# Performance work log

Hardware: AMD Instinct MI355X
Metric: run time of the kernel (lower is better)

The kernel has to match this reference:

```python
import jax, jax.numpy as jnp
import numpy as np
from itertools import combinations

WIRES, LAYERS, CUTOFF, OUT_WIRES, BATCH = 4, 2, 10, 3, 2048

def _annih(c):
    # annihilation operator a in the Fock basis, truncated to cutoff c
    return jnp.diag(jnp.sqrt(jnp.arange(1, c, dtype=jnp.float32)), 1).astype(jnp.complex64)

_expm = jnp.vectorize(jax.scipy.linalg.expm, signature='(n,n)->(n,n)')

def _squeeze(r, phi, a):
    # S(z) = exp((z* a^2 - z a+^2)/2), z = r e^{i phi}; r, phi have arbitrary batch shape
    z = (r * jnp.exp(1j * phi)).astype(jnp.complex64)[..., None, None]
    a2 = a @ a
    ad2 = a.conj().T @ a.conj().T
    return _expm(0.5 * (jnp.conj(z) * a2 - z * ad2))

def _disp(r, phi, a):
    # D(alpha) = exp(alpha a+ - alpha* a), alpha = r e^{i phi}
    al = (r * jnp.exp(1j * phi)).astype(jnp.complex64)[..., None, None]
    ad = a.conj().T
    return _expm(al * ad - jnp.conj(al) * a)

def _bs(theta, phi, a):
    # SF BSgate: B = exp(theta (e^{i phi} a b+ - e^{-i phi} a+ b))
    ad = a.conj().T
    G = theta * (jnp.exp(1j * phi) * jnp.kron(a, ad) - jnp.exp(-1j * phi) * jnp.kron(ad, a))
    return jax.scipy.linalg.expm(G.astype(jnp.complex64))

def _cx(s, a):
    # SF CXgate: exp(-i s x1 p2 / hbar) = exp(-(s/2) (a+a+) kron (b-b+)) with hbar=2
    ad = a.conj().T
    G = (-s / 2.0) * jnp.kron(a + ad, a - ad)
    return jax.scipy.linalg.expm(G.astype(jnp.complex64))

def _apply1(state, U, m):
    # apply single-mode gate U ([c,c] shared or [B,c,c] per-sample) to mode m
    if U.ndim == 2:
        return jnp.moveaxis(jnp.tensordot(state, U, axes=[[1 + m], [1]]), -1, 1 + m)
    st = jnp.moveaxis(state, 1 + m, -1)
    st = jnp.einsum('b...j,bij->b...i', st, U)
    return jnp.moveaxis(st, -1, 1 + m)

def _apply2(state, U4, m1, m2):
    # apply two-mode gate U4 [c,c,c,c] (out1,out2,in1,in2) to modes (m1, m2)
    st = jnp.moveaxis(state, (1 + m1, 1 + m2), (-2, -1))
    st = jnp.einsum('b...kl,ijkl->b...ij', st, U4)
    return jnp.moveaxis(st, (-2, -1), (1 + m1, 1 + m2))

def _forward(jets, s_scale, disp_mag, disp_phase, squeeze_mag, squeeze_phase, w_dense, b_dense):
    B, c = jets.shape[0], CUTOFF
    a = _annih(c)
    eta, phi, pt = jets[:, :, 0], jets[:, :, 1], jets[:, :, 2]  # each [B, WIRES]
    scale = 10.0 / (1.0 + jnp.exp(-s_scale)) + 0.01
    # vacuum |0...0> for every sample
    state = jnp.zeros((B,) + (c,) * WIRES, jnp.complex64)
    state = state.at[(slice(None),) + (0,) * WIRES].set(1.0)
    # per-sample data-encoding gates
    S_enc = _squeeze(eta, pt * phi / 2.0, a)      # [B, WIRES, c, c]
    D_enc = _disp(scale * pt, eta, a)             # [B, WIRES, c, c]
    for w in range(WIRES):
        state = _apply1(state, S_enc[:, w], w)
        state = _apply1(state, D_enc[:, w], w)
    # fixed entangling gates (shared across batch)
    CX = _cx(1.0, a).reshape(c, c, c, c)
    BS = _bs(jnp.pi / 4.0, jnp.pi / 2.0, a).reshape(c, c, c, c)
    # learned per-layer single-mode gates (shared across batch)
    S_lay = _squeeze(squeeze_mag, squeeze_phase, a)  # [LAYERS, WIRES, c, c]
    D_lay = _disp(disp_mag, disp_phase, a)
    for L in range(LAYERS):
        for (i, j) in combinations(range(WIRES), 2):
            state = _apply2(state, CX, i, j)
        for i in range(WIRES):
            state = _apply2(state, BS, i, (i + 1) % WIRES)
        for w in range(WIRES):
            state = _apply1(state, S_lay[L, w], w)
            state = _apply1(state, D_lay[L, w], w)
    probs = jnp.abs(state) ** 2
    nvec = jnp.arange(c, dtype=jnp.float32)
    photons = jnp.stack(
        [probs.sum(axis=tuple(1 + k for k in range(WIRES) if k != m)) @ nvec
         for m in range(OUT_WIRES)], axis=1)  # [B, OUT_WIRES] mean photon numbers
    return (photons @ w_dense + b_dense)[:, 0]  # [B]

def setup_inputs() -> dict:
    key = jax.random.key(0)
    ks = jax.random.split(key, 8)
    u = lambda k, sh: jax.random.uniform(k, sh, jnp.float32, -1.0, 1.0)
    return {
        'jets': 0.3 * jax.random.normal(ks[0], (BATCH, WIRES, 3), jnp.float32),
        's_scale': u(ks[1], ()),
        'disp_mag': u(ks[2], (LAYERS, WIRES)),
        'disp_phase': u(ks[3], (LAYERS, WIRES)),
        'squeeze_mag': u(ks[4], (LAYERS, WIRES)),
        'squeeze_phase': u(ks[5], (LAYERS, WIRES)),
        'w_dense': u(ks[6], (OUT_WIRES, 1)),
        'b_dense': jnp.zeros((1,), jnp.float32),
    }

def reference(jets, s_scale, disp_mag, disp_phase, squeeze_mag, squeeze_phase, w_dense, b_dense):
    return _forward(jets, s_scale, disp_mag, disp_phase, squeeze_mag, squeeze_phase, w_dense, b_dense)
```

## Files before the change

kernel.cpp:

```cpp
#include <hip/hip_runtime.h>
#include <math.h>


namespace {

constexpr int NTB = 1024;
constexpr int SMEM_STATE = 162352;
constexpr double THETA = 0.7853981633974483096;

struct cxf { float x, y; };
typedef float v2f __attribute__((ext_vector_type(2)));
typedef float v4f __attribute__((ext_vector_type(4)));

constexpr int U_OFF = 15872;

__device__ __forceinline__ cxf gen_squeeze_f(int i, int j, float zr, float zi){
  if (j == i+2){ float g = 0.5f*sqrtf((float)((i+1)*(i+2))); return {zr*g, -zi*g}; }
  if (i == j+2){ float g = 0.5f*sqrtf((float)((j+1)*(j+2))); return {-zr*g, -zi*g}; }
  return {0.f, 0.f};
}
__device__ __forceinline__ cxf gen_disp_f(int i, int j, float ar, float ai){
  if (i == j+1){ float g = sqrtf((float)i); return {ar*g, ai*g}; }
  if (j == i+1){ float g = sqrtf((float)j); return {-ar*g, ai*g}; }
  return {0.f, 0.f};
}

__device__ void expm_f32(bool act, int n, cxf* M, cxf* P, cxf* T, cxf* R, int lane){
  const int n2 = n*n;
  if (act){
    for (int e=lane; e<n2; e+=64){ M[e].x *= 0x1p-10f; M[e].y *= 0x1p-10f; }
    for (int e=lane; e<n2; e+=64){
      P[e] = M[e];
      cxf r = M[e];
      if (e % (n+1) == 0) r.x += 1.f;
      R[e] = r;
    }
  }
  __syncthreads();
  for (int t=2; t<=12; ++t){
    if (act){
      float inv = 1.f/(float)t;
      for (int e=lane; e<n2; e+=64){
        int i = e/n, j = e - i*n;
        float ax=0.f, ay=0.f;
        for (int k=0;k<n;k++){
          cxf p = P[i*n+k], m = M[k*n+j];
          ax += p.x*m.x - p.y*m.y;
          ay += p.x*m.y + p.y*m.x;
        }
        T[e] = {ax*inv, ay*inv};
      }
    }
    __syncthreads();
    { cxf* tmp = P; P = T; T = tmp; }
    if (act){ for (int e=lane; e<n2; e+=64){ R[e].x += P[e].x; R[e].y += P[e].y; } }
    __syncthreads();
  }
  for (int s=0; s<10; ++s){
    if (act){
      for (int e=lane; e<n2; e+=64){
        int i = e/n, j = e - i*n;
        float ax=0.f, ay=0.f;
        for (int k=0;k<n;k++){
          cxf p = R[i*n+k], q = R[k*n+j];
          ax += p.x*q.x - p.y*q.y;
          ay += p.x*q.y + p.y*q.x;
        }
        T[e] = {ax, ay};
      }
    }
    __syncthreads();
    { cxf* tmp = R; R = T; T = tmp; }
    __syncthreads();
  }
}

__global__ __launch_bounds__(256)
void gates_kernel(const float* __restrict__ dmag, const float* __restrict__ dphase,
                  const float* __restrict__ smag, const float* __restrict__ sphase,
                  float* __restrict__ wsf){
  __shared__ double lam[10];
  __shared__ float scr[4][4][200];
  const int tid = threadIdx.x;
  const int wv = tid >> 6, lane = tid & 63, g = blockIdx.x;
  float* ws_V  = wsf;
  float* ws_VT = wsf + 100;
  float* ws_W  = wsf + 200;
  cxf* ws_BS   = (cxf*)(wsf + 1200);
  cxf* ws_stage= (cxf*)(wsf + 6600);

  if (tid < 10){
    double lo = -6.0, hi = 6.0;
    for (int it=0; it<80; ++it){
      double mid = 0.5*(lo+hi);
      int cnt = 0; double q = 1.0;
      for (int i=0;i<10;i++){
        q = -mid - (i ? (double)i/q : 0.0);
        if (fabs(q) < 1e-300) q = -1e-300;
        if (q < 0.0) cnt++;
      }
      if (cnt > tid) hi = mid; else lo = mid;
    }
    double x = 0.5*(lo+hi);
    double p[10];
    p[0] = 1.0; p[1] = x;
    for (int k=1;k<9;k++) p[k+1] = (x*p[k] - sqrt((double)k)*p[k-1]) * (1.0/sqrt((double)(k+1)));
    double nn=0.0; for (int k=0;k<10;k++) nn += p[k]*p[k];
    double inv = 1.0/sqrt(nn);
    lam[tid] = x;
    if (g == 0){
      for (int k=0;k<10;k++){
        float v = (float)(p[k]*inv);
        ws_V[k*10+tid]  = v;
        ws_VT[tid*10+k] = v;
      }
    }
  }
  __syncthreads();

  int t = g*4 + wv;
  bool act = (t < 45);
  int n = 10, bn = 0, ilo = 0;
  if (act && t >= 10 && t < 29){
    bn = t - 10; ilo = bn < 10 ? 0 : bn - 9;
    int ihi = bn < 10 ? bn : 9;
    n = ihi - ilo + 1;
  }
  cxf* M = (cxf*)scr[wv][0];
  cxf* P = (cxf*)scr[wv][1];
  cxf* T = (cxf*)scr[wv][2];
  cxf* R = (cxf*)scr[wv][3];
  if (act){
    if (t < 10){
      float l = (float)lam[t];
      for (int e=lane; e<100; e+=64){
        int i=e/10, j=e-10*i;
        float v = 0.f;
        if (j == i+1) v = -0.5f*l*sqrtf((float)(i+1));
        else if (i == j+1) v = 0.5f*l*sqrtf((float)i);
        M[e] = {v, 0.f};
      }
    } else if (t < 29){
      for (int e=lane; e<n*n; e+=64){
        int rr=e/n, c=e-n*rr;
        float v = 0.f;
        if (c == rr+1) v = (float)THETA*sqrtf((float)((ilo+rr+1)*(bn-ilo-rr)));
        else if (rr == c+1) v = (float)THETA*sqrtf((float)((ilo+c+1)*(bn-ilo-c)));
        M[e] = {0.f, v};
      }
    } else {
      int idx = t-29, kind = idx>>3, L=(idx>>2)&1, w=idx&3;
      float r_ = kind ? dmag[L*4+w]   : smag[L*4+w];
      float ph = kind ? dphase[L*4+w] : sphase[L*4+w];
      float zr = r_*cosf(ph), zi = r_*sinf(ph);
      for (int e=lane; e<100; e+=64){
        int i=e/10, j=e-10*i;
        M[e] = kind ? gen_disp_f(i,j,zr,zi) : gen_squeeze_f(i,j,zr,zi);
      }
    }
  }
  __syncthreads();
  expm_f32(act, n, M, P, T, R, lane);
  if (act){
    if (t < 10){
      for (int e=lane;e<100;e+=64){
        int i=e/10, j=e-10*i;
        ws_W[t*100 + j*10 + i] = R[e].x;
      }
    } else if (t < 29){
      for (int e=lane;e<100;e+=64){
        int rr=e/10, c=e-10*rr;
        cxf o; o.x=0.f; o.y=0.f;
        if (rr < n && c < n) o = R[rr*n+c];
        ws_BS[bn*100 + c*10 + rr] = o;
      }
    } else {
      int idx = t-29;
      for (int e=lane;e<100;e+=64) ws_stage[idx*100 + e] = R[e];
    }
  }
}

__global__ __launch_bounds__(512)
void fuse_kernel(float* __restrict__ wsf){
  __shared__ cxf ulraw[8][100];
  const int tid = threadIdx.x, wv = tid>>6, lane = tid&63;
  const cxf* stage = (const cxf*)(wsf + 6600);
  cxf* ws_UL = (cxf*)(wsf + 5000);
  cxf* ws_WU = (cxf*)(wsf + 9800);
  const float* V  = wsf;
  const float* Wt = wsf + 200;
  const cxf* Sm = stage + wv*100;
  const cxf* Dm = stage + (8+wv)*100;
  for (int e=lane; e<100; e+=64){
    int i=e/10, j=e-10*i;
    float ax=0.f, ay=0.f;
    for (int k=0;k<10;k++){
      cxf d=Dm[i*10+k], s=Sm[k*10+j];
      ax += d.x*s.x - d.y*s.y;
      ay += d.x*s.y + d.y*s.x;
    }
    ulraw[wv][e] = {ax, ay};
  }
  __syncthreads();
  cxf t0={0.f,0.f}, t1={0.f,0.f};
  if (wv == 0){
    {
      int e=lane, i=e/10, j=e-10*i;
      float ox=0.f, oy=0.f;
      for (int k=0;k<10;k++){ float v=V[k*10+i]; ox+=v*ulraw[0][k*10+j].x; oy+=v*ulraw[0][k*10+j].y; }
      t0 = {ox, oy};
    }
    if (lane+64 < 100){
      int e=lane+64, i=e/10, j=e-10*i;
      float ox=0.f, oy=0.f;
      for (int k=0;k<10;k++){ float v=V[k*10+i]; ox+=v*ulraw[0][k*10+j].x; oy+=v*ulraw[0][k*10+j].y; }
      t1 = {ox, oy};
    }
  }
  __syncthreads();
  if (wv == 0){
    ulraw[0][lane] = t0;
    if (lane+64 < 100) ulraw[0][lane+64] = t1;
  }
  __syncthreads();
  for (int e=tid; e<400; e+=512){
    int fi = e/100, r = e-100*fi;
    int f = (fi==0) ? 0 : (3+fi);
    int i=r/10, j=r-10*i;
    ws_UL[f*100 + j*10 + i] = ulraw[f][i*10+j];
  }
  for (int round=0; round<4; ++round){
    int id = round*8 + wv;
    if (id < 30){
      int b = 1 + id/10, n = id - (id/10)*10;
      const cxf* Ub = ulraw[b];
      for (int e=lane; e<100; e+=64){
        int i=e/10, j=e-10*i;
        float ax=0.f, ay=0.f;
        for (int k=0;k<10;k++){
          float w = Wt[n*100 + k*10 + i];
          ax += w*Ub[k*10+j].x;
          ay += w*Ub[k*10+j].y;
        }
        cxf o; o.x=ax; o.y=ay;
        ws_WU[id*100 + j*10 + i] = o;
      }
    }
  }
}

__global__ __launch_bounds__(128)
void enc_kernel(const float* __restrict__ jets, const float* __restrict__ sscale,
                float* __restrict__ wsf){
  __shared__ float scr[2][4][200];
  __shared__ cxf col[10];
  __shared__ cxf uacc[10];
  const int tid = threadIdx.x, wv = tid>>6, lane = tid&63;
  const int blk = blockIdx.x, b = blk>>2, w = blk&3;

  float eta = jets[b*12 + w*3 + 0];
  float jph = jets[b*12 + w*3 + 1];
  float pt  = jets[b*12 + w*3 + 2];

  cxf* M = (cxf*)scr[wv][0];
  cxf* P = (cxf*)scr[wv][1];
  cxf* T = (cxf*)scr[wv][2];
  cxf* R = (cxf*)scr[wv][3];
  {
    float zr, zi;
    if (wv == 0){ float phs = pt*jph*0.5f; zr = eta*cosf(phs); zi = eta*sinf(phs); }
    else {
      double sc = 10.0/(1.0 + exp(-(double)sscale[0])) + 0.01;
      float mag = (float)sc*pt; zr = mag*cosf(eta); zi = mag*sinf(eta);
    }
    for (int e=lane; e<100; e+=64){
      int i=e/10, j=e-10*i;
      M[e] = wv ? gen_disp_f(i,j,zr,zi) : gen_squeeze_f(i,j,zr,zi);
    }
  }
  __syncthreads();
  expm_f32(true, 10, M, P, T, R, lane);
  cxf* Rs = (cxf*)scr[0][3];
  cxf* Rd = (cxf*)scr[1][3];
  if (tid < 10) col[tid] = Rs[tid*10];
  __syncthreads();
  if (tid < 10){
    float ax=0.f, ay=0.f;
    for (int k=0;k<10;k++){
      cxf d = Rd[tid*10+k], c = col[k];
      ax += d.x*c.x - d.y*c.y;
      ay += d.x*c.y + d.y*c.x;
    }
    uacc[tid] = {ax, ay};
  }
  __syncthreads();
  if (tid < 10){
    float rx, ry;
    if (w == 0){
      rx = 0.f; ry = 0.f;
      for (int k=0;k<10;k++){
        float v = wsf[k*10 + tid];
        rx += v*uacc[k].x;
        ry += v*uacc[k].y;
      }
    } else { rx = uacc[tid].x; ry = uacc[tid].y; }
    float* u_out = wsf + U_OFF + (b*40 + w*10 + tid)*2;
    u_out[0] = rx;
    u_out[1] = ry;
  }
}

__device__ __forceinline__ constexpr int WS(int w){
  return w==0 ? 1010 : (w==1 ? 101 : (w==2 ? 10 : 1));
}

#define DECL_ACC4 \
  v4f a0={0.f,0.f,0.f,0.f}, a1=a0, a2=a0, a3=a0, a4=a0, \
      a5=a0, a6=a0, a7=a0, a8=a0, a9=a0;

#define LDS_RD10 \
  v4f r0=S[base], r1=S[base+sm], r2=S[base+2*sm], r3=S[base+3*sm], r4=S[base+4*sm], \
      r5=S[base+5*sm], r6=S[base+6*sm], r7=S[base+7*sm], r8=S[base+8*sm], r9=S[base+9*sm];

#define CE(i,ur,ui) \
  a##i = __builtin_elementwise_fma((v4f){(ur),(ur),(ur),(ur)}, vv, a##i); \
  a##i = __builtin_elementwise_fma((v4f){-(ui),(ui),-(ui),(ui)}, vs, a##i);
#define RE(i,u) a##i = __builtin_elementwise_fma((v4f){(u),(u),(u),(u)}, vv, a##i);

#define CSTEP(rk,krow) { \
  const v4f* Up = (const v4f*)(U + (krow)*10); \
  v4f q0=Up[0],q1=Up[1],q2=Up[2],q3=Up[3],q4=Up[4]; \
  v4f vv=rk, vs=__builtin_shufflevector(rk,rk,1,0,3,2); \
  CE(0,q0.x,q0.y) CE(1,q0.z,q0.w) CE(2,q1.x,q1.y) CE(3,q1.z,q1.w) \
  CE(4,q2.x,q2.y) CE(5,q2.z,q2.w) CE(6,q3.x,q3.y) CE(7,q3.z,q3.w) \
  CE(8,q4.x,q4.y) CE(9,q4.z,q4.w) }
#define CSTEP_ALL CSTEP(r0,0) CSTEP(r1,1) CSTEP(r2,2) CSTEP(r3,3) CSTEP(r4,4) \
  CSTEP(r5,5) CSTEP(r6,6) CSTEP(r7,7) CSTEP(r8,8) CSTEP(r9,9)

#define RSTEP2(ra_,rb_,krow) { \
  const v4f* Mp = (const v4f*)(Mt + (krow)*10); \
  v4f q0=Mp[0],q1=Mp[1],q2=Mp[2],q3=Mp[3],q4=Mp[4]; \
  { v4f vv=ra_; RE(0,q0.x) RE(1,q0.y) RE(2,q0.z) RE(3,q0.w) RE(4,q1.x) \
                RE(5,q1.y) RE(6,q1.z) RE(7,q1.w) RE(8,q2.x) RE(9,q2.y) } \
  { v4f vv=rb_; RE(0,q2.z) RE(1,q2.w) RE(2,q3.x) RE(3,q3.y) RE(4,q3.z) \
                RE(5,q3.w) RE(6,q4.x) RE(7,q4.y) RE(8,q4.z) RE(9,q4.w) } }
#define RSTEP_ALL RSTEP2(r0,r1,0) RSTEP2(r2,r3,2) RSTEP2(r4,r5,4) \
  RSTEP2(r6,r7,6) RSTEP2(r8,r9,8)

#define PST4(i) { S[base + (i)*sm] = a##i; }
#define PALL4 PST4(0) PST4(1) PST4(2) PST4(3) PST4(4) PST4(5) PST4(6) PST4(7) PST4(8) PST4(9)
#define BSTQ(r) if ((r) < sz){ S[wadr] = a##r; wadr += ds; }
#define BSTQ_ALL BSTQ(0) BSTQ(1) BSTQ(2) BSTQ(3) BSTQ(4) BSTQ(5) BSTQ(6) BSTQ(7) BSTQ(8) BSTQ(9)

__device__ __forceinline__ void apply1_c4(v4f* S, const cxf* __restrict__ U, int m, int tid){
  const int sm = WS(m);
  const int x0 = (m==0)?1:0, x1=(m<=1)?2:1, x2=(m<=2)?3:2;
  const int s0 = WS(x0), s1 = WS(x1), s2 = WS(x2);
  if (tid < 1000){
    int c0=tid/100, rem=tid-100*c0, c1=rem/10, c2=rem-10*c1;
    int base = c0*s0 + c1*s1 + c2*s2;
    LDS_RD10
    DECL_ACC4
    CSTEP_ALL
    PALL4
  }
}

__device__ __forceinline__ void apply1_r4(v4f* S, const float* __restrict__ Mt, int m, int tid){
  const int sm = WS(m);
  const int x0 = (m==0)?1:0, x1=(m<=1)?2:1, x2=(m<=2)?3:2;
  const int s0 = WS(x0), s1 = WS(x1), s2 = WS(x2);
  if (tid < 1000){
    int c0=tid/100, rem=tid-100*c0, c1=rem/10, c2=rem-10*c1;
    int base = c0*s0 + c1*s1 + c2*s2;
    LDS_RD10
    DECL_ACC4
    RSTEP_ALL
    PALL4
  }
}

__device__ __forceinline__ void applyW4(v4f* S, const float* __restrict__ Wall, int m1, int m2, int tid){
  const int sm  = WS(m2);
  const int sm1 = WS(m1);
  int ra=-1, rb=-1;
  for (int q=0;q<4;q++) if (q!=m1 && q!=m2){ if (ra<0) ra=q; else rb=q; }
  const int sa = WS(ra), sb = WS(rb);
  if (tid < 1000){
    int n = tid/100, rem = tid-100*n, qa = rem/10, qb = rem-10*qa;
    int base = n*sm1 + qa*sa + qb*sb;
    const float* __restrict__ Mt = Wall + n*100;
    LDS_RD10
    DECL_ACC4
    RSTEP_ALL
    PALL4
  }
}

__device__ __forceinline__ void applyWU4(v4f* S, const cxf* __restrict__ WUall, int m2, int tid){
  const int sm = WS(m2);
  const int ra = (m2==1)?2:1;
  const int rb = (m2==3)?2:3;
  const int sa = WS(ra), sb = WS(rb);
  if (tid < 1000){
    int n = tid/100, rem = tid-100*n, qa = rem/10, qb = rem-10*qa;
    int base = n*WS(0) + qa*sa + qb*sb;
    const cxf* __restrict__ U = WUall + n*100;
    LDS_RD10
    DECL_ACC4
    CSTEP_ALL
    PALL4
  }
}

__device__ __forceinline__ v2f measure14(const v4f* S, const cxf* __restrict__ U, int m, int tid){
  const int sm = WS(m);
  const int x0 = (m==0)?1:0, x1=(m<=1)?2:1, x2=3;
  const int s0 = WS(x0), s1 = WS(x1), s2 = WS(x2);
  v2f s = {0.f, 0.f};
  if (tid < 1000){
    int c0=tid/100, rem=tid-100*c0, c1=rem/10, c2=rem-10*c1;
    int base = c0*s0 + c1*s1 + c2*s2;
    LDS_RD10
    DECL_ACC4
    CSTEP_ALL
    #define MQ4(i) { s.x += (float)(i)*(a##i.x*a##i.x + a##i.y*a##i.y); \
                     s.y += (float)(i)*(a##i.z*a##i.z + a##i.w*a##i.w); }
    MQ4(1) MQ4(2) MQ4(3) MQ4(4) MQ4(5) MQ4(6) MQ4(7) MQ4(8) MQ4(9)
    #undef MQ4
  }
  return s;
}

__device__ __forceinline__ void applyBS4(v4f* S, const cxf* __restrict__ BSp, int m1, int m2, int tid){
  int ra=-1, rb=-1;
  for (int q=0;q<4;q++) if (q!=m1 && q!=m2){ if (ra<0) ra=q; else rb=q; }
  const int sa = WS(ra), sb = WS(rb);
  const int s1 = WS(m1), s2 = WS(m2);
  const int ds = s1 - s2;
  #pragma unroll 1
  for (int w0=0; w0<2048; w0+=NTB){
    int it = w0 + tid;
    if (it < 1900){
      int bn = it/100, rest = it-100*bn;
      int ilo = bn<10?0:bn-9, ihi = bn<10?bn:9, sz = ihi-ilo+1;
      int ca = rest/10, cb = rest-10*ca;
      int base = ca*sa + cb*sb;
      const cxf* __restrict__ Bt = BSp + bn*100;
      DECL_ACC4
      int radr = base + ilo*s1 + (bn-ilo)*s2;
      int kk = 0;
      #pragma unroll 1
      for (int c=0;c<sz;c++){
        v4f vv = S[radr];
        v4f vs = __builtin_shufflevector(vv, vv, 1, 0, 3, 2);
        const v4f* Bp = (const v4f*)(Bt + kk);
        v4f q0=Bp[0],q1=Bp[1],q2=Bp[2],q3=Bp[3],q4=Bp[4];
        CE(0,q0.x,q0.y) CE(1,q0.z,q0.w) CE(2,q1.x,q1.y) CE(3,q1.z,q1.w)
        CE(4,q2.x,q2.y) CE(5,q2.z,q2.w) CE(6,q3.x,q3.y) CE(7,q3.z,q3.w)
        CE(8,q4.x,q4.y) CE(9,q4.z,q4.w)
        radr += ds; kk += 10;
      }
      int wadr = base + ilo*s1 + (bn-ilo)*s2;
      BSTQ_ALL
    }
  }
}

__global__ __launch_bounds__(NTB)
__attribute__((amdgpu_waves_per_eu(4)))
void state_kernel(const float* __restrict__ wd, const float* __restrict__ bd,
                  const float* __restrict__ wsf, float* __restrict__ out){
  extern __shared__ __align__(16) char smem[];
  v4f* S    = (v4f*)smem;
  cxf* uv   = (cxf*)(smem + 161584);
  v2f* red  = (v2f*)(smem + 162224);

  const float* __restrict__ V   = wsf;
  const float* __restrict__ VT  = wsf + 100;
  const float* __restrict__ W   = wsf + 200;
  const cxf*   __restrict__ BSm = (const cxf*)(wsf + 1200);
  const cxf*   __restrict__ UL  = (const cxf*)(wsf + 5000);
  const cxf*   __restrict__ WU  = (const cxf*)(wsf + 9800);
  const cxf*   __restrict__ uw  = (const cxf*)(wsf + U_OFF);

  const int tid = threadIdx.x, wv = tid>>6, lane = tid&63;
  const int b = blockIdx.x;

  if (tid < 80) uv[tid] = uw[b*80 + tid];
  __syncthreads();

  for (int e=tid; e<10000; e+=NTB){
    int c0=e/1000, r_=e-1000*c0, c1=r_/100, r2_=r_-100*c1, c2=r2_/10, c3=r2_-10*c2;
    cxf A0 = uv[c0],    B0 = uv[10+c1], C0 = uv[20+c2], D0 = uv[30+c3];
    cxf A1 = uv[40+c0], B1 = uv[50+c1], C1 = uv[60+c2], D1 = uv[70+c3];
    float pr = A0.x*B0.x - A0.y*B0.y, pi = A0.x*B0.y + A0.y*B0.x;
    float qr = pr*C0.x - pi*C0.y,  qi = pr*C0.y + pi*C0.x;
    float e0r = qr*D0.x - qi*D0.y, e0i = qr*D0.y + qi*D0.x;
    pr = A1.x*B1.x - A1.y*B1.y; pi = A1.x*B1.y + A1.y*B1.x;
    qr = pr*C1.x - pi*C1.y;  qi = pr*C1.y + pi*C1.x;
    float e1r = qr*D1.x - qi*D1.y, e1i = qr*D1.y + qi*D1.x;
    S[c0*1010 + c1*101 + c2*10 + c3] = (v4f){e0r, e0i, e1r, e1i};
  }
  __syncthreads();

  applyW4(S, W, 0, 1, tid); __syncthreads();
  applyW4(S, W, 0, 2, tid); __syncthreads();
  applyW4(S, W, 0, 3, tid); __syncthreads();
  apply1_r4(S, VT, 0, tid); __syncthreads();
  apply1_r4(S, V, 1, tid);  __syncthreads();
  applyW4(S, W, 1, 2, tid); __syncthreads();
  applyW4(S, W, 1, 3, tid); __syncthreads();
  apply1_r4(S, VT, 1, tid); __syncthreads();
  apply1_r4(S, V, 2, tid);  __syncthreads();
  applyW4(S, W, 2, 3, tid); __syncthreads();
  apply1_r4(S, VT, 2, tid); __syncthreads();
  applyBS4(S, BSm, 0, 1, tid); __syncthreads();
  applyBS4(S, BSm, 1, 2, tid); __syncthreads();
  applyBS4(S, BSm, 2, 3, tid); __syncthreads();
  applyBS4(S, BSm, 3, 0, tid); __syncthreads();
  apply1_c4(S, UL, 0, tid); __syncthreads();

  applyWU4(S, WU,        1, tid); __syncthreads();
  applyWU4(S, WU + 1000, 2, tid); __syncthreads();
  applyWU4(S, WU + 2000, 3, tid); __syncthreads();
  apply1_r4(S, VT, 0, tid); __syncthreads();
  apply1_r4(S, V, 1, tid);  __syncthreads();
  applyW4(S, W, 1, 2, tid); __syncthreads();
  applyW4(S, W, 1, 3, tid); __syncthreads();
  apply1_r4(S, VT, 1, tid); __syncthreads();
  apply1_r4(S, V, 2, tid);  __syncthreads();
  applyW4(S, W, 2, 3, tid); __syncthreads();
  apply1_r4(S, VT, 2, tid); __syncthreads();
  applyBS4(S, BSm, 0, 1, tid); __syncthreads();
  applyBS4(S, BSm, 1, 2, tid); __syncthreads();
  applyBS4(S, BSm, 2, 3, tid); __syncthreads();
  applyBS4(S, BSm, 3, 0, tid); __syncthreads();

  float w0 = wd[0], w1 = wd[1], w2 = wd[2];
  v2f m0 = measure14(S, UL + 400, 0, tid);
  v2f m1 = measure14(S, UL + 500, 1, tid);
  v2f m2 = measure14(S, UL + 600, 2, tid);
  v2f acc;
  acc.x = w0*m0.x + w1*m1.x + w2*m2.x;
  acc.y = w0*m0.y + w1*m1.y + w2*m2.y;

  for (int off=32; off; off>>=1){
    acc.x += __shfl_down(acc.x, off, 64);
    acc.y += __shfl_down(acc.y, off, 64);
  }
  if (lane == 0) red[wv] = acc;
  __syncthreads();
  if (tid == 0){
    float sx = 0.f, sy = 0.f;
    for (int i=0;i<16;i++){ sx += red[i].x; sy += red[i].y; }
    out[2*b+0] = sx + bd[0];
    out[2*b+1] = sy + bd[0];
  }
}

}

extern "C" void kernel_launch(void* const* d_in, const int* in_sizes, int n_in,
                              void* d_out, int out_size, void* d_ws, size_t ws_size,
                              hipStream_t stream){
  const float* jets   = (const float*)d_in[0];
  const float* sscale = (const float*)d_in[1];
  const float* dmag   = (const float*)d_in[2];
  const float* dphase = (const float*)d_in[3];
  const float* smag   = (const float*)d_in[4];
  const float* sphase = (const float*)d_in[5];
  const float* wd     = (const float*)d_in[6];
  const float* bd     = (const float*)d_in[7];
  float* out = (float*)d_out;
  float* wsf = (float*)d_ws;
  int B = in_sizes[0] / 12;

  (void)hipFuncSetAttribute(reinterpret_cast<const void*>(&state_kernel),
                            hipFuncAttributeMaxDynamicSharedMemorySize, SMEM_STATE);

  gates_kernel<<<12, 256, 0, stream>>>(dmag, dphase, smag, sphase, wsf);
  fuse_kernel<<<1, 512, 0, stream>>>(wsf);
  enc_kernel<<<B*4, 128, 0, stream>>>(jets, sscale, wsf);
  state_kernel<<<B/2, NTB, SMEM_STATE, stream>>>(wd, bd, wsf, out);
}
```

Measured before the change: 856.7 us.

## Halve block size and give each thread two state fibers

After: 930.4 us. 1.09x slower.

```diff
diff --git a/kernel.cpp b/kernel.cpp
--- a/kernel.cpp
+++ b/kernel.cpp
@@ -4,7 +4,7 @@
 
 namespace {
 
-constexpr int NTB = 1024;
+constexpr int NTB = 512;
 constexpr int SMEM_STATE = 162352;
 constexpr double THETA = 0.7853981633974483096;
 
@@ -315,55 +315,108 @@
   return w==0 ? 1010 : (w==1 ? 101 : (w==2 ? 10 : 1));
 }
 
-#define DECL_ACC4 \
-  v4f a0={0.f,0.f,0.f,0.f}, a1=a0, a2=a0, a3=a0, a4=a0, \
-      a5=a0, a6=a0, a7=a0, a8=a0, a9=a0;
-
-#define LDS_RD10 \
-  v4f r0=S[base], r1=S[base+sm], r2=S[base+2*sm], r3=S[base+3*sm], r4=S[base+4*sm], \
-      r5=S[base+5*sm], r6=S[base+6*sm], r7=S[base+7*sm], r8=S[base+8*sm], r9=S[base+9*sm];
-
-#define CE(i,ur,ui) \
+#define SHUF4(v) __builtin_shufflevector(v, v, 1, 0, 3, 2)
+
+#define DECL_A \
+  v4f a0={0.f,0.f,0.f,0.f}, a1=a0, a2=a0, a3=a0, a4=a0, a5=a0, a6=a0, a7=a0, a8=a0, a9=a0;
+#define DECL_B \
+  v4f b0={0.f,0.f,0.f,0.f}, b1=b0, b2=b0, b3=b0, b4=b0, b5=b0, b6=b0, b7=b0, b8=b0, b9=b0;
+
+#define CE_A(i,ur,ui) \
   a##i = __builtin_elementwise_fma((v4f){(ur),(ur),(ur),(ur)}, vv, a##i); \
   a##i = __builtin_elementwise_fma((v4f){-(ui),(ui),-(ui),(ui)}, vs, a##i);
-#define RE(i,u) a##i = __builtin_elementwise_fma((v4f){(u),(u),(u),(u)}, vv, a##i);
-
-#define CSTEP(rk,krow) { \
+#define CE_B(i,ur,ui) \
+  b##i = __builtin_elementwise_fma((v4f){(ur),(ur),(ur),(ur)}, vv, b##i); \
+  b##i = __builtin_elementwise_fma((v4f){-(ui),(ui),-(ui),(ui)}, vs, b##i);
+#define RE_A(i,u) a##i = __builtin_elementwise_fma((v4f){(u),(u),(u),(u)}, vv, a##i);
+#define RE_B(i,u) b##i = __builtin_elementwise_fma((v4f){(u),(u),(u),(u)}, vv, b##i);
+
+#define CROW_A CE_A(0,q0.x,q0.y) CE_A(1,q0.z,q0.w) CE_A(2,q1.x,q1.y) CE_A(3,q1.z,q1.w) \
+  CE_A(4,q2.x,q2.y) CE_A(5,q2.z,q2.w) CE_A(6,q3.x,q3.y) CE_A(7,q3.z,q3.w) \
+  CE_A(8,q4.x,q4.y) CE_A(9,q4.z,q4.w)
+#define CROW_B CE_B(0,q0.x,q0.y) CE_B(1,q0.z,q0.w) CE_B(2,q1.x,q1.y) CE_B(3,q1.z,q1.w) \
+  CE_B(4,q2.x,q2.y) CE_B(5,q2.z,q2.w) CE_B(6,q3.x,q3.y) CE_B(7,q3.z,q3.w) \
+  CE_B(8,q4.x,q4.y) CE_B(9,q4.z,q4.w)
+
+#define RROWS_A(ra_,rb_) \
+  { { v4f vv=ra_; RE_A(0,q0.x) RE_A(1,q0.y) RE_A(2,q0.z) RE_A(3,q0.w) RE_A(4,q1.x) \
+                  RE_A(5,q1.y) RE_A(6,q1.z) RE_A(7,q1.w) RE_A(8,q2.x) RE_A(9,q2.y) } \
+    { v4f vv=rb_; RE_A(0,q2.z) RE_A(1,q2.w) RE_A(2,q3.x) RE_A(3,q3.y) RE_A(4,q3.z) \
+                  RE_A(5,q3.w) RE_A(6,q4.x) RE_A(7,q4.y) RE_A(8,q4.z) RE_A(9,q4.w) } }
+#define RROWS_B(ga_,gb_) \
+  { { v4f vv=ga_; RE_B(0,q0.x) RE_B(1,q0.y) RE_B(2,q0.z) RE_B(3,q0.w) RE_B(4,q1.x) \
+                  RE_B(5,q1.y) RE_B(6,q1.z) RE_B(7,q1.w) RE_B(8,q2.x) RE_B(9,q2.y) } \
+    { v4f vv=gb_; RE_B(0,q2.z) RE_B(1,q2.w) RE_B(2,q3.x) RE_B(3,q3.y) RE_B(4,q3.z) \
+                  RE_B(5,q3.w) RE_B(6,q4.x) RE_B(7,q4.y) RE_B(8,q4.z) RE_B(9,q4.w) } }
+
+#define CSTEP2U(rk,gk,krow) { \
   const v4f* Up = (const v4f*)(U + (krow)*10); \
   v4f q0=Up[0],q1=Up[1],q2=Up[2],q3=Up[3],q4=Up[4]; \
-  v4f vv=rk, vs=__builtin_shufflevector(rk,rk,1,0,3,2); \
-  CE(0,q0.x,q0.y) CE(1,q0.z,q0.w) CE(2,q1.x,q1.y) CE(3,q1.z,q1.w) \
-  CE(4,q2.x,q2.y) CE(5,q2.z,q2.w) CE(6,q3.x,q3.y) CE(7,q3.z,q3.w) \
-  CE(8,q4.x,q4.y) CE(9,q4.z,q4.w) }
-#define CSTEP_ALL CSTEP(r0,0) CSTEP(r1,1) CSTEP(r2,2) CSTEP(r3,3) CSTEP(r4,4) \
-  CSTEP(r5,5) CSTEP(r6,6) CSTEP(r7,7) CSTEP(r8,8) CSTEP(r9,9)
-
-#define RSTEP2(ra_,rb_,krow) { \
+  { v4f vv=rk, vs=SHUF4(rk); CROW_A } \
+  { v4f vv=gk, vs=SHUF4(gk); CROW_B } }
+#define CALL2U CSTEP2U(r0,g0,0) CSTEP2U(r1,g1,1) CSTEP2U(r2,g2,2) CSTEP2U(r3,g3,3) \
+  CSTEP2U(r4,g4,4) CSTEP2U(r5,g5,5) CSTEP2U(r6,g6,6) CSTEP2U(r7,g7,7) \
+  CSTEP2U(r8,g8,8) CSTEP2U(r9,g9,9)
+
+#define CSTEP1A(rk,krow) { \
+  const v4f* Up = (const v4f*)(U1 + (krow)*10); \
+  v4f q0=Up[0],q1=Up[1],q2=Up[2],q3=Up[3],q4=Up[4]; \
+  v4f vv=rk, vs=SHUF4(rk); CROW_A }
+#define CSTEP1B(gk,krow) { \
+  const v4f* Up = (const v4f*)(U2 + (krow)*10); \
+  v4f q0=Up[0],q1=Up[1],q2=Up[2],q3=Up[3],q4=Up[4]; \
+  v4f vv=gk, vs=SHUF4(gk); CROW_B }
+#define CALL_COND CSTEP1A(r0,0) CSTEP1B(g0,0) CSTEP1A(r1,1) CSTEP1B(g1,1) \
+  CSTEP1A(r2,2) CSTEP1B(g2,2) CSTEP1A(r3,3) CSTEP1B(g3,3) \
+  CSTEP1A(r4,4) CSTEP1B(g4,4) CSTEP1A(r5,5) CSTEP1B(g5,5) \
+  CSTEP1A(r6,6) CSTEP1B(g6,6) CSTEP1A(r7,7) CSTEP1B(g7,7) \
+  CSTEP1A(r8,8) CSTEP1B(g8,8) CSTEP1A(r9,9) CSTEP1B(g9,9)
+
+#define RSTEP2U(rka,rkb,gka,gkb,krow) { \
   const v4f* Mp = (const v4f*)(Mt + (krow)*10); \
   v4f q0=Mp[0],q1=Mp[1],q2=Mp[2],q3=Mp[3],q4=Mp[4]; \
-  { v4f vv=ra_; RE(0,q0.x) RE(1,q0.y) RE(2,q0.z) RE(3,q0.w) RE(4,q1.x) \
-                RE(5,q1.y) RE(6,q1.z) RE(7,q1.w) RE(8,q2.x) RE(9,q2.y) } \
-  { v4f vv=rb_; RE(0,q2.z) RE(1,q2.w) RE(2,q3.x) RE(3,q3.y) RE(4,q3.z) \
-                RE(5,q3.w) RE(6,q4.x) RE(7,q4.y) RE(8,q4.z) RE(9,q4.w) } }
-#define RSTEP_ALL RSTEP2(r0,r1,0) RSTEP2(r2,r3,2) RSTEP2(r4,r5,4) \
-  RSTEP2(r6,r7,6) RSTEP2(r8,r9,8)
-
-#define PST4(i) { S[base + (i)*sm] = a##i; }
-#define PALL4 PST4(0) PST4(1) PST4(2) PST4(3) PST4(4) PST4(5) PST4(6) PST4(7) PST4(8) PST4(9)
-#define BSTQ(r) if ((r) < sz){ S[wadr] = a##r; wadr += ds; }
-#define BSTQ_ALL BSTQ(0) BSTQ(1) BSTQ(2) BSTQ(3) BSTQ(4) BSTQ(5) BSTQ(6) BSTQ(7) BSTQ(8) BSTQ(9)
+  RROWS_A(rka,rkb) RROWS_B(gka,gkb) }
+#define RALL_U RSTEP2U(r0,r1,g0,g1,0) RSTEP2U(r2,r3,g2,g3,2) RSTEP2U(r4,r5,g4,g5,4) \
+  RSTEP2U(r6,r7,g6,g7,6) RSTEP2U(r8,r9,g8,g9,8)
+
+#define RSTEP2A(rka,rkb,krow) { \
+  const v4f* Mp = (const v4f*)(Mt1 + (krow)*10); \
+  v4f q0=Mp[0],q1=Mp[1],q2=Mp[2],q3=Mp[3],q4=Mp[4]; \
+  RROWS_A(rka,rkb) }
+#define RSTEP2B(gka,gkb,krow) { \
+  const v4f* Mp = (const v4f*)(Mt2 + (krow)*10); \
+  v4f q0=Mp[0],q1=Mp[1],q2=Mp[2],q3=Mp[3],q4=Mp[4]; \
+  RROWS_B(gka,gkb) }
+#define RALL_COND RSTEP2A(r0,r1,0) RSTEP2B(g0,g1,0) RSTEP2A(r2,r3,2) RSTEP2B(g2,g3,2) \
+  RSTEP2A(r4,r5,4) RSTEP2B(g4,g5,4) RSTEP2A(r6,r7,6) RSTEP2B(g6,g7,6) \
+  RSTEP2A(r8,r9,8) RSTEP2B(g8,g9,8)
+
+#define RD_A v4f r0=S[base1], r1=S[base1+sm], r2=S[base1+2*sm], r3=S[base1+3*sm], \
+  r4=S[base1+4*sm], r5=S[base1+5*sm], r6=S[base1+6*sm], r7=S[base1+7*sm], \
+  r8=S[base1+8*sm], r9=S[base1+9*sm];
+#define RD_B v4f g0=S[base2], g1=S[base2+sm], g2=S[base2+2*sm], g3=S[base2+3*sm], \
+  g4=S[base2+4*sm], g5=S[base2+5*sm], g6=S[base2+6*sm], g7=S[base2+7*sm], \
+  g8=S[base2+8*sm], g9=S[base2+9*sm];
+
+#define ST_A { S[base1]=a0; S[base1+sm]=a1; S[base1+2*sm]=a2; S[base1+3*sm]=a3; \
+  S[base1+4*sm]=a4; S[base1+5*sm]=a5; S[base1+6*sm]=a6; S[base1+7*sm]=a7; \
+  S[base1+8*sm]=a8; S[base1+9*sm]=a9; }
+#define ST_B { S[base2]=b0; S[base2+sm]=b1; S[base2+2*sm]=b2; S[base2+3*sm]=b3; \
+  S[base2+4*sm]=b4; S[base2+5*sm]=b5; S[base2+6*sm]=b6; S[base2+7*sm]=b7; \
+  S[base2+8*sm]=b8; S[base2+9*sm]=b9; }
 
 __device__ __forceinline__ void apply1_c4(v4f* S, const cxf* __restrict__ U, int m, int tid){
   const int sm = WS(m);
   const int x0 = (m==0)?1:0, x1=(m<=1)?2:1, x2=(m<=2)?3:2;
   const int s0 = WS(x0), s1 = WS(x1), s2 = WS(x2);
-  if (tid < 1000){
+  if (tid < 500){
     int c0=tid/100, rem=tid-100*c0, c1=rem/10, c2=rem-10*c1;
-    int base = c0*s0 + c1*s1 + c2*s2;
-    LDS_RD10
-    DECL_ACC4
-    CSTEP_ALL
-    PALL4
+    int base1 = c0*s0 + c1*s1 + c2*s2;
+    int base2 = base1 + 5*s0;
+    RD_A RD_B
+    DECL_A DECL_B
+    CALL2U
+    ST_A ST_B
   }
 }
 
@@ -371,13 +424,14 @@
   const int sm = WS(m);
   const int x0 = (m==0)?1:0, x1=(m<=1)?2:1, x2=(m<=2)?3:2;
   const int s0 = WS(x0), s1 = WS(x1), s2 = WS(x2);
-  if (tid < 1000){
+  if (tid < 500){
     int c0=tid/100, rem=tid-100*c0, c1=rem/10, c2=rem-10*c1;
-    int base = c0*s0 + c1*s1 + c2*s2;
-    LDS_RD10
-    DECL_ACC4
-    RSTEP_ALL
-    PALL4
+    int base1 = c0*s0 + c1*s1 + c2*s2;
+    int base2 = base1 + 5*s0;
+    RD_A RD_B
+    DECL_A DECL_B
+    RALL_U
+    ST_A ST_B
   }
 }
 
@@ -386,15 +440,19 @@
   const int sm1 = WS(m1);
   int ra=-1, rb=-1;
   for (int q=0;q<4;q++) if (q!=m1 && q!=m2){ if (ra<0) ra=q; else rb=q; }
-  const int sa = WS(ra), sb = WS(rb);
-  if (tid < 1000){
+  const int sa0 = WS(ra), sb0 = WS(rb);
+  const bool sw = (sa0==101 && sb0==10);
+  const int sa = sw ? sb0 : sa0, sb = sw ? sa0 : sb0;
+  if (tid < 500){
     int n = tid/100, rem = tid-100*n, qa = rem/10, qb = rem-10*qa;
-    int base = n*sm1 + qa*sa + qb*sb;
-    const float* __restrict__ Mt = Wall + n*100;
-    LDS_RD10
-    DECL_ACC4
-    RSTEP_ALL
-    PALL4
+    int base1 = n*sm1 + qa*sa + qb*sb;
+    int base2 = base1 + 5*sm1;
+    const float* __restrict__ Mt1 = Wall + n*100;
+    const float* __restrict__ Mt2 = Wall + (n+5)*100;
+    RD_A RD_B
+    DECL_A DECL_B
+    RALL_COND
+    ST_A ST_B
   }
 }
 
@@ -402,15 +460,19 @@
   const int sm = WS(m2);
   const int ra = (m2==1)?2:1;
   const int rb = (m2==3)?2:3;
-  const int sa = WS(ra), sb = WS(rb);
-  if (tid < 1000){
+  const int sa0 = WS(ra), sb0 = WS(rb);
+  const bool sw = (sa0==101 && sb0==10);
+  const int sa = sw ? sb0 : sa0, sb = sw ? sa0 : sb0;
+  if (tid < 500){
     int n = tid/100, rem = tid-100*n, qa = rem/10, qb = rem-10*qa;
-    int base = n*WS(0) + qa*sa + qb*sb;
-    const cxf* __restrict__ U = WUall + n*100;
-    LDS_RD10
-    DECL_ACC4
-    CSTEP_ALL
-    PALL4
+    int base1 = n*WS(0) + qa*sa + qb*sb;
+    int base2 = base1 + 5*WS(0);
+    const cxf* __restrict__ U1 = WUall + n*100;
+    const cxf* __restrict__ U2 = WUall + (n+5)*100;
+    RD_A RD_B
+    DECL_A DECL_B
+    CALL_COND
+    ST_A ST_B
   }
 }
 
@@ -419,14 +481,16 @@
   const int x0 = (m==0)?1:0, x1=(m<=1)?2:1, x2=3;
   const int s0 = WS(x0), s1 = WS(x1), s2 = WS(x2);
   v2f s = {0.f, 0.f};
-  if (tid < 1000){
+  if (tid < 500){
     int c0=tid/100, rem=tid-100*c0, c1=rem/10, c2=rem-10*c1;
-    int base = c0*s0 + c1*s1 + c2*s2;
-    LDS_RD10
-    DECL_ACC4
-    CSTEP_ALL
-    #define MQ4(i) { s.x += (float)(i)*(a##i.x*a##i.x + a##i.y*a##i.y); \
-                     s.y += (float)(i)*(a##i.z*a##i.z + a##i.w*a##i.w); }
+    int base1 = c0*s0 + c1*s1 + c2*s2;
+    int base2 = base1 + 5*s0;
+    RD_A RD_B
+    DECL_A DECL_B
+    CALL2U
+    #define MQ4(i) { \
+      s.x += (float)(i)*(a##i.x*a##i.x + a##i.y*a##i.y + b##i.x*b##i.x + b##i.y*b##i.y); \
+      s.y += (float)(i)*(a##i.z*a##i.z + a##i.w*a##i.w + b##i.z*b##i.z + b##i.w*b##i.w); }
     MQ4(1) MQ4(2) MQ4(3) MQ4(4) MQ4(5) MQ4(6) MQ4(7) MQ4(8) MQ4(9)
     #undef MQ4
   }
@@ -436,7 +500,9 @@
 __device__ __forceinline__ void applyBS4(v4f* S, const cxf* __restrict__ BSp, int m1, int m2, int tid){
   int ra=-1, rb=-1;
   for (int q=0;q<4;q++) if (q!=m1 && q!=m2){ if (ra<0) ra=q; else rb=q; }
-  const int sa = WS(ra), sb = WS(rb);
+  const int sa0 = WS(ra), sb0 = WS(rb);
+  const bool sw = (sa0==101 && sb0==10);
+  const int sa = sw ? sb0 : sa0, sb = sw ? sa0 : sb0;
   const int s1 = WS(m1), s2 = WS(m2);
   const int ds = s1 - s2;
   #pragma unroll 1
@@ -448,28 +514,30 @@
       int ca = rest/10, cb = rest-10*ca;
       int base = ca*sa + cb*sb;
       const cxf* __restrict__ Bt = BSp + bn*100;
-      DECL_ACC4
+      DECL_A
       int radr = base + ilo*s1 + (bn-ilo)*s2;
       int kk = 0;
       #pragma unroll 1
       for (int c=0;c<sz;c++){
-        v4f vv = S[radr];
-        v4f vs = __builtin_shufflevector(vv, vv, 1, 0, 3, 2);
+        v4f rk = S[radr];
         const v4f* Bp = (const v4f*)(Bt + kk);
         v4f q0=Bp[0],q1=Bp[1],q2=Bp[2],q3=Bp[3],q4=Bp[4];
-        CE(0,q0.x,q0.y) CE(1,q0.z,q0.w) CE(2,q1.x,q1.y) CE(3,q1.z,q1.w)
-        CE(4,q2.x,q2.y) CE(5,q2.z,q2.w) CE(6,q3.x,q3.y) CE(7,q3.z,q3.w)
-        CE(8,q4.x,q4.y) CE(9,q4.z,q4.w)
+        v4f vv=rk, vs=SHUF4(rk);
+        CROW_A
         radr += ds; kk += 10;
       }
       int wadr = base + ilo*s1 + (bn-ilo)*s2;
-      BSTQ_ALL
+      { if (0 < sz){ S[wadr]=a0; wadr+=ds; } if (1 < sz){ S[wadr]=a1; wadr+=ds; }
+        if (2 < sz){ S[wadr]=a2; wadr+=ds; } if (3 < sz){ S[wadr]=a3; wadr+=ds; }
+        if (4 < sz){ S[wadr]=a4; wadr+=ds; } if (5 < sz){ S[wadr]=a5; wadr+=ds; }
+        if (6 < sz){ S[wadr]=a6; wadr+=ds; } if (7 < sz){ S[wadr]=a7; wadr+=ds; }
+        if (8 < sz){ S[wadr]=a8; wadr+=ds; } if (9 < sz){ S[wadr]=a9; wadr+=ds; } }
     }
   }
 }
 
 __global__ __launch_bounds__(NTB)
-__attribute__((amdgpu_waves_per_eu(4)))
+__attribute__((amdgpu_waves_per_eu(2)))
 void state_kernel(const float* __restrict__ wd, const float* __restrict__ bd,
                   const float* __restrict__ wsf, float* __restrict__ out){
   extern __shared__ __align__(16) char smem[];
@@ -554,7 +622,7 @@
   __syncthreads();
   if (tid == 0){
     float sx = 0.f, sy = 0.f;
-    for (int i=0;i<16;i++){ sx += red[i].x; sy += red[i].y; }
+    for (int i=0;i<8;i++){ sx += red[i].x; sy += red[i].y; }
     out[2*b+0] = sx + bd[0];
     out[2*b+1] = sy + bd[0];
   }
```
